# Performance work log

Hardware: AMD Instinct MI355X
Metric: run time of the kernel (lower is better)

Reference implementation:

```python
import jax, jax.numpy as jnp
import numpy as np

EPS = 1e-06
MAX_R = 18.0
TINY = 1e-15

D_MODEL = 512
H = 8
N_SP = 32          # spatial_dim per head
A = N_SP + 1       # Lorentz ambient dim
TAU = 1.0
KARCHER_STEPS = 1
B, T = 2, 512


def minkowski_inner(x, y):
    # <x,y>_L = -x0*y0 + sum_i xi*yi
    return -x[..., 0] * y[..., 0] + jnp.sum(x[..., 1:] * y[..., 1:], axis=-1)


def project_to_hyperboloid(x):
    xx = jnp.maximum(jnp.abs(minkowski_inner(x, x)), TINY)
    y = x / jnp.sqrt(xx)[..., None]
    return jnp.concatenate([jnp.abs(y[..., :1]), y[..., 1:]], axis=-1)


def FL(z):
    # Euclidean param z in R^n -> Lorentz point in H^n (R^{n+1})
    r = jnp.linalg.norm(z, axis=-1, keepdims=True)
    r_safe = jnp.clip(r, 1e-12, MAX_R)
    s = z / r_safe
    y = jnp.concatenate([jnp.cosh(r_safe), jnp.sinh(r_safe) * s], axis=-1)
    return project_to_hyperboloid(y)


def safe_acosh(z):
    return jnp.arccosh(jnp.maximum(z, 1.0 + EPS))


def log_map(p, y):
    alpha = -minkowski_inner(p, y)                       # (...,)
    dist = safe_acosh(alpha)[..., None]                  # (...,1)
    u = y + alpha[..., None] * p
    un = jnp.sqrt(jnp.maximum(minkowski_inner(u, u), TINY))[..., None]
    return (dist / jnp.maximum(un, TINY)) * u


def exp_map(p, v):
    vn = jnp.sqrt(jnp.maximum(minkowski_inner(v, v), TINY))[..., None]
    y = jnp.cosh(vn) * p + (jnp.sinh(vn) / jnp.maximum(vn, TINY)) * v
    return project_to_hyperboloid(y)


def _forward(x, Wq, bq, Wk, bk, Wv, bv, Wo, bo):
    Bx, Tx, _ = x.shape

    def lift(W, b):
        z = x @ W.T + b                                   # (B,T,H*n)
        return z.reshape(Bx, Tx, H, N_SP).transpose(0, 2, 1, 3)  # (B,H,T,n)

    Q = FL(lift(Wq, bq))                                  # (B,H,T,A)
    K = FL(lift(Wk, bk))
    V = FL(lift(Wv, bv))

    # pairwise hyperbolic distance: -<Q_i,K_j>_L = Q0*K0 - spatial dot
    ip = (jnp.einsum('bhi,bhj->bhij', Q[..., 0], K[..., 0])
          - jnp.einsum('bhia,bhja->bhij', Q[..., 1:], K[..., 1:]))
    d = safe_acosh(ip)                                    # (B,H,T,T)
    scores = -TAU * d * d
    attn = jax.nn.softmax(scores, axis=-1)                # (B,H,T,T)

    # Karcher-mean aggregation of V around Y (init at Q)
    Y = Q
    for _ in range(KARCHER_STEPS):
        logv = log_map(Y[:, :, :, None, :], V[:, :, None, :, :])  # (B,H,T,T,A)
        u = jnp.einsum('bhij,bhija->bhia', attn, logv)            # (B,H,T,A)
        Y = exp_map(Y, u)

    # log-map at origin anchor, project to d_model
    Y_bTHA = Y.transpose(0, 2, 1, 3)                      # (B,T,H,A)
    p0 = jnp.zeros((A,), dtype=Y.dtype).at[0].set(1.0)    # Lorentz origin
    Z_tan = log_map(jnp.broadcast_to(p0, Y_bTHA.shape), Y_bTHA)
    Z_tan = Z_tan.reshape(Bx, Tx, H * A)
    Z = Z_tan @ Wo.T + bo                                 # (B,T,d_model)
    return Z


def setup_inputs() -> dict:
    key = jax.random.key(0)
    ks = jax.random.split(key, 9)
    sc = 0.02
    return {
        'x':  jax.random.normal(ks[0], (B, T, D_MODEL), dtype=jnp.float32),
        'Wq': jax.random.normal(ks[1], (H * N_SP, D_MODEL), dtype=jnp.float32) * sc,
        'bq': jnp.zeros((H * N_SP,), dtype=jnp.float32),
        'Wk': jax.random.normal(ks[2], (H * N_SP, D_MODEL), dtype=jnp.float32) * sc,
        'bk': jnp.zeros((H * N_SP,), dtype=jnp.float32),
        'Wv': jax.random.normal(ks[3], (H * N_SP, D_MODEL), dtype=jnp.float32) * sc,
        'bv': jnp.zeros((H * N_SP,), dtype=jnp.float32),
        'Wo': jax.random.normal(ks[4], (D_MODEL, H * A), dtype=jnp.float32) * sc,
        'bo': jnp.zeros((D_MODEL,), dtype=jnp.float32),
    }


def reference(x, Wq, bq, Wk, bk, Wv, bv, Wo, bo):
    return _forward(x, Wq, bq, Wk, bk, Wv, bv, Wo, bo)
```

## Files before the change

### kernel.cpp

```cpp
#include <hip/hip_runtime.h>
#include <math.h>


namespace {

constexpr int Tq = 512;
constexpr int QS = 36;

#define EPSF  1e-6f
#define CINV  3.16227766e7f

using short8 = __attribute__((ext_vector_type(8))) short;
using f32x4  = __attribute__((ext_vector_type(4))) float;

__device__ __forceinline__ float facosh(float x) {
    return __logf(x + __builtin_amdgcn_sqrtf(fmaf(x, x, -1.0f)));
}

__device__ __forceinline__ void cvt_hilo(float x, unsigned short& h, unsigned short& l) {
    const unsigned u = __float_as_uint(x);
    h = (unsigned short)(u >> 16);
    const float xh = __uint_as_float(u & 0xFFFF0000u);
    l = (unsigned short)(__float_as_uint(x - xh) >> 16);
}

__device__ __forceinline__ unsigned short cvt_rne(float x) {
    const unsigned u = __float_as_uint(x);
    return (unsigned short)((u + 0x7FFFu + ((u >> 16) & 1u)) >> 16);
}

__device__ __forceinline__ uint4 pack8(const unsigned short* s) {
    uint4 r;
    r.x = (unsigned)s[0] | ((unsigned)s[1] << 16);
    r.y = (unsigned)s[2] | ((unsigned)s[3] << 16);
    r.z = (unsigned)s[4] | ((unsigned)s[5] << 16);
    r.w = (unsigned)s[6] | ((unsigned)s[7] << 16);
    return r;
}

__global__ __launch_bounds__(256) void gemm_qkv_mfma_kernel(
    const float* __restrict__ x,
    const float* __restrict__ Wq, const float* __restrict__ bq,
    const float* __restrict__ Wk, const float* __restrict__ bk,
    const float* __restrict__ Wv, const float* __restrict__ bv,
    float* __restrict__ Qf, unsigned short* __restrict__ Qh,
    unsigned short* __restrict__ Kh,
    unsigned short* __restrict__ Vh, unsigned short* __restrict__ V2h)
{
    __shared__ unsigned short Ah[16][72];
    __shared__ unsigned short Bh[64][72];
    __shared__ float sT[16][65];

    const int bid = blockIdx.y * 12 + blockIdx.x;
    const int swz = (bid & 7) * 96 + (bid >> 3);
    const int n0 = (swz >> 6) * 64;
    const int m0 = (swz & 63) * 16;

    const int t  = threadIdx.x;
    const int l  = t & 63, w = t >> 6;
    const int wc = w * 16;
    const int fr = l & 15, fk = (l >> 4) * 8;

    const int arow = t >> 4, akseg = (t & 15) * 4;
    const int brow = t >> 2, bkseg = (t & 3) * 16;
    const int ob  = n0 + brow;
    const float* WselB = (ob < 256) ? Wq : (ob < 512 ? Wk : Wv);
    const int obr = ob & 255;

    f32x4 acc = (f32x4){0.f, 0.f, 0.f, 0.f};

    for (int k0 = 0; k0 < 512; k0 += 64) {
        {
            const float4 av = *reinterpret_cast<const float4*>(
                &x[(m0 + arow) * 512 + k0 + akseg]);
            uint2 H;
            H.x = (unsigned)cvt_rne(av.x) | ((unsigned)cvt_rne(av.y) << 16);
            H.y = (unsigned)cvt_rne(av.z) | ((unsigned)cvt_rne(av.w) << 16);
            *reinterpret_cast<uint2*>(&Ah[arow][akseg]) = H;

            const float* wp = WselB + obr * 512 + k0 + bkseg;
            unsigned short hh[16];
            #pragma unroll
            for (int c = 0; c < 4; ++c) {
                const float4 v = *reinterpret_cast<const float4*>(wp + c * 4);
                hh[c*4+0] = cvt_rne(v.x); hh[c*4+1] = cvt_rne(v.y);
                hh[c*4+2] = cvt_rne(v.z); hh[c*4+3] = cvt_rne(v.w);
            }
            *reinterpret_cast<uint4*>(&Bh[brow][bkseg])     = pack8(hh);
            *reinterpret_cast<uint4*>(&Bh[brow][bkseg + 8]) = pack8(hh + 8);
        }
        __syncthreads();

        #pragma unroll
        for (int ks = 0; ks < 2; ++ks) {
            const int kb = ks * 32 + fk;
            const short8 ah = *reinterpret_cast<const short8*>(&Ah[fr][kb]);
            const short8 bh = *reinterpret_cast<const short8*>(&Bh[wc + fr][kb]);
            acc = __builtin_amdgcn_mfma_f32_16x16x32_bf16(ah, bh, acc, 0, 0, 0);
        }
        __syncthreads();
    }

    #pragma unroll
    for (int r = 0; r < 4; ++r)
        sT[(l >> 4) * 4 + r][wc + fr] = acc[r];
    __syncthreads();

    if (t < 32) {
        const int m = t >> 1, half = t & 1;
        const int row = m0 + m;
        const int b = row >> 9, tt = row & 511;
        const int which = n0 >> 8;
        const int h = ((n0 & 255) >> 5) + half;
        const int bh2 = b * 8 + h;
        const float* bsel = (which == 0) ? bq : (which == 1 ? bk : bv);

        float ys[32];
        float s2 = 0.f;
        #pragma unroll
        for (int k = 0; k < 32; ++k) {
            ys[k] = sT[m][half * 32 + k] + bsel[h * 32 + k];
            s2 = fmaf(ys[k], ys[k], s2);
        }
        const float rr = __builtin_amdgcn_sqrtf(s2);
        const float rs = fminf(fmaxf(rr, 1e-12f), 18.0f);
        const float e  = __expf(rs);
        const float ei = __builtin_amdgcn_rcpf(e);
        const float ch = 0.5f * (e + ei);
        float sc = 0.5f * (e - ei) / rs;
        if (rs < 1e-3f) sc = fmaf(rs * rs, 1.0f / 6.0f, 1.0f);
        float y0 = ch;
        float mink = -y0 * y0;
        #pragma unroll
        for (int k = 0; k < 32; ++k) { ys[k] *= sc; mink = fmaf(ys[k], ys[k], mink); }
        const float inv = __builtin_amdgcn_rsqf(fmaxf(fabsf(mink), 1e-15f));
        y0 = fabsf(y0 * inv);

        const long rbase = (long)(bh2 * Tq + tt) * 64;
        unsigned short hbuf[64];
        #pragma unroll
        for (int k = 33; k < 64; ++k) hbuf[k] = 0;

        if (which == 0) {
            float* qp = Qf + (bh2 * Tq + tt) * QS;
            #pragma unroll
            for (int c = 0; c < 8; ++c) {
                float4 v4;
                v4.x = ys[c*4+0] * inv; v4.y = ys[c*4+1] * inv;
                v4.z = ys[c*4+2] * inv; v4.w = ys[c*4+3] * inv;
                *reinterpret_cast<float4*>(qp + c * 4) = v4;
                hbuf[c*4+0] = cvt_rne(v4.x); hbuf[c*4+1] = cvt_rne(v4.y);
                hbuf[c*4+2] = cvt_rne(v4.z); hbuf[c*4+3] = cvt_rne(v4.w);
            }
            float4 tail; tail.x = y0; tail.y = 0.f; tail.z = 0.f; tail.w = 0.f;
            *reinterpret_cast<float4*>(qp + 32) = tail;
            hbuf[32] = cvt_rne(y0);
            #pragma unroll
            for (int c = 0; c < 8; ++c)
                *reinterpret_cast<uint4*>(&Qh[rbase + c * 8]) = pack8(hbuf + c * 8);
        } else if (which == 1) {
            #pragma unroll
            for (int k = 0; k < 32; ++k)
                hbuf[k] = cvt_rne(-ys[k] * inv);
            hbuf[32] = cvt_rne(y0);
            #pragma unroll
            for (int c = 0; c < 8; ++c)
                *reinterpret_cast<uint4*>(&Kh[rbase + c * 8]) = pack8(hbuf + c * 8);
        } else {
            const long v2b = (long)bh2 * 48 * Tq + tt;
            #pragma unroll
            for (int k = 0; k < 32; ++k) {
                const float v = ys[k] * inv;
                hbuf[k] = cvt_rne(-v);
                V2h[v2b + (1 + k) * Tq] = cvt_rne(v);
            }
            hbuf[32] = cvt_rne(y0);
            V2h[v2b] = cvt_rne(y0);
            #pragma unroll
            for (int c = 0; c < 8; ++c)
                *reinterpret_cast<uint4*>(&Vh[rbase + c * 8]) = pack8(hbuf + c * 8);
        }
    }
}

__global__ __launch_bounds__(512) void attn_mfma_kernel(
    const float* __restrict__ Qf, const unsigned short* __restrict__ Qh,
    const unsigned short* __restrict__ Kh,
    const unsigned short* __restrict__ Vh, const unsigned short* __restrict__ V2h,
    float* __restrict__ Ztan)
{
    __shared__ unsigned short sPh[16][528];
    __shared__ float sSe[8][16];
    __shared__ float sWp[2][16][48];

    const int bid = blockIdx.y * 32 + blockIdx.x;
    const int swz = (bid & 7) * 64 + (bid >> 3);
    const int bh = swz >> 5;
    const int i0 = (swz & 31) * 16;

    const int t  = threadIdx.x;
    const int l  = t & 63, w = t >> 6;
    const int fr = l & 15, fk = (l >> 4) * 8;

    short8 qh[2];
    {
        const long qb = (long)(bh * Tq + i0 + fr) * 64;
        #pragma unroll
        for (int ks = 0; ks < 2; ++ks)
            qh[ks] = *reinterpret_cast<const short8*>(&Qh[qb + ks * 32 + fk]);
    }

    float seLoc[4] = {0.f, 0.f, 0.f, 0.f};
    #pragma unroll
    for (int c = 0; c < 4; ++c) {
        const int j0 = (w * 4 + c) * 16;
        const long kb = (long)(bh * Tq + j0 + fr) * 64;
        f32x4 aK = (f32x4){0.f, 0.f, 0.f, 0.f};
        f32x4 aV = (f32x4){0.f, 0.f, 0.f, 0.f};
        #pragma unroll
        for (int ks = 0; ks < 2; ++ks) {
            const long o = kb + ks * 32 + fk;
            const short8 bkh = *reinterpret_cast<const short8*>(&Kh[o]);
            const short8 bvh = *reinterpret_cast<const short8*>(&Vh[o]);
            aK = __builtin_amdgcn_mfma_f32_16x16x32_bf16(qh[ks], bkh, aK, 0, 0, 0);
            aV = __builtin_amdgcn_mfma_f32_16x16x32_bf16(qh[ks], bvh, aV, 0, 0, 0);
        }
        #pragma unroll
        for (int r = 0; r < 4; ++r) {
            const int i = (l >> 4) * 4 + r;
            const int j = j0 + fr;
            const float d  = facosh(fmaxf(aK[r], 1.0f + EPSF));
            const float al = fmaxf(aV[r], 1.0f + EPSF);
            const float e  = __expf(-d * d);
            const float p  = e * facosh(al);
            seLoc[r] += e;
            sPh[i][j] = cvt_rne(p);
        }
    }
    #pragma unroll
    for (int r = 0; r < 4; ++r) {
        float v = seLoc[r];
        v += __shfl_xor(v, 1, 64);
        v += __shfl_xor(v, 2, 64);
        v += __shfl_xor(v, 4, 64);
        v += __shfl_xor(v, 8, 64);
        if ((l & 15) == 0) sSe[w][(l >> 4) * 4 + r] = v;
    }
    __syncthreads();

    if (w < 6) {
        const int a0  = (w % 3) * 16;
        const int kh2 = w / 3;
        const long vb = (long)bh * 48 * Tq + (long)(a0 + fr) * Tq;
        f32x4 aW = (f32x4){0.f, 0.f, 0.f, 0.f};
        #pragma unroll 4
        for (int ks = kh2 * 8; ks < kh2 * 8 + 8; ++ks) {
            const int ko = ks * 32 + fk;
            const short8 ph  = *reinterpret_cast<const short8*>(&sPh[fr][ko]);
            const short8 v2h = *reinterpret_cast<const short8*>(&V2h[vb + ko]);
            aW = __builtin_amdgcn_mfma_f32_16x16x32_bf16(ph, v2h, aW, 0, 0, 0);
        }
        #pragma unroll
        for (int r = 0; r < 4; ++r)
            sWp[kh2][(l >> 4) * 4 + r][a0 + fr] = aW[r];
    }
    __syncthreads();

    if (t < 16) {
        const int i = t;
        float seT = 0.f;
        #pragma unroll
        for (int ww = 0; ww < 8; ++ww) seT += sSe[ww][i];
        float W[33];
        #pragma unroll
        for (int a = 0; a < 33; ++a) W[a] = sWp[0][i][a] + sWp[1][i][a];
        const float* qrow = Qf + (long)(bh * Tq + i0 + i) * QS;
        const float q0 = qrow[32];
        float dot = 0.f;
        #pragma unroll
        for (int a = 1; a < 33; ++a) dot = fmaf(qrow[a - 1], W[a], dot);
        const float S = q0 * W[0] - dot;
        const float cs = CINV * __builtin_amdgcn_rcpf(seT);
        const float y0 = fmaf(cs, fmaf(S, q0, W[0]), q0);
        float mink = -y0 * y0;
        float yv[32];
        #pragma unroll
        for (int a = 1; a < 33; ++a) {
            const float qa = qrow[a - 1];
            const float ya = fmaf(cs, fmaf(S, qa, W[a]), qa);
            yv[a - 1] = ya;
            mink = fmaf(ya, ya, mink);
        }
        const float inv = __builtin_amdgcn_rsqf(fmaxf(fabsf(mink), 1e-15f));
        const float Y0 = fabsf(y0 * inv);
        const float dist0 = facosh(fmaxf(Y0, 1.0f + EPSF));
        const float coef = dist0 * CINV;
        const int b = bh >> 3, h = bh & 7;
        float* zp = Ztan + ((b * Tq + (i0 + i)) * 264) + h * 33;
        zp[0] = coef * (2.0f * Y0);
        #pragma unroll
        for (int a = 1; a < 33; ++a) zp[a] = coef * (yv[a - 1] * inv);
    }
}

__global__ __launch_bounds__(256) void out_gemm_mfma_kernel(
    const float* __restrict__ Ztan, const float* __restrict__ Wo,
    const float* __restrict__ bo, float* __restrict__ out)
{
    __shared__ unsigned short Ah[32][72], Al[32][72];
    __shared__ unsigned short Bh[32][72], Bl[32][72];

    const int n0 = blockIdx.x * 32;
    const int m0 = blockIdx.y * 32;
    const int t  = threadIdx.x;
    const int l  = t & 63, w = t >> 6;
    const int wr = (w >> 1) * 16, wc = (w & 1) * 16;
    const int fr = l & 15, fk = (l >> 4) * 8;

    const int sr = t >> 3, sk = (t & 7) * 8;

    f32x4 acc = (f32x4){0.f, 0.f, 0.f, 0.f};

    for (int k0 = 0; k0 < 264; k0 += 64) {
        const bool full = (k0 + sk + 7 < 264);
        {
            unsigned short h8[8], l8[8];
            if (full) {
                const float4 a0v = *reinterpret_cast<const float4*>(
                    &Ztan[(m0 + sr) * 264 + k0 + sk]);
                const float4 a1v = *reinterpret_cast<const float4*>(
                    &Ztan[(m0 + sr) * 264 + k0 + sk + 4]);
                cvt_hilo(a0v.x, h8[0], l8[0]); cvt_hilo(a0v.y, h8[1], l8[1]);
                cvt_hilo(a0v.z, h8[2], l8[2]); cvt_hilo(a0v.w, h8[3], l8[3]);
                cvt_hilo(a1v.x, h8[4], l8[4]); cvt_hilo(a1v.y, h8[5], l8[5]);
                cvt_hilo(a1v.z, h8[6], l8[6]); cvt_hilo(a1v.w, h8[7], l8[7]);
            } else {
                #pragma unroll
                for (int c = 0; c < 8; ++c) { h8[c] = 0; l8[c] = 0; }
            }
            *reinterpret_cast<uint4*>(&Ah[sr][sk]) = pack8(h8);
            *reinterpret_cast<uint4*>(&Al[sr][sk]) = pack8(l8);

            if (full) {
                const float4 b0v = *reinterpret_cast<const float4*>(
                    &Wo[(n0 + sr) * 264 + k0 + sk]);
                const float4 b1v = *reinterpret_cast<const float4*>(
                    &Wo[(n0 + sr) * 264 + k0 + sk + 4]);
                cvt_hilo(b0v.x, h8[0], l8[0]); cvt_hilo(b0v.y, h8[1], l8[1]);
                cvt_hilo(b0v.z, h8[2], l8[2]); cvt_hilo(b0v.w, h8[3], l8[3]);
                cvt_hilo(b1v.x, h8[4], l8[4]); cvt_hilo(b1v.y, h8[5], l8[5]);
                cvt_hilo(b1v.z, h8[6], l8[6]); cvt_hilo(b1v.w, h8[7], l8[7]);
            } else {
                #pragma unroll
                for (int c = 0; c < 8; ++c) { h8[c] = 0; l8[c] = 0; }
            }
            *reinterpret_cast<uint4*>(&Bh[sr][sk]) = pack8(h8);
            *reinterpret_cast<uint4*>(&Bl[sr][sk]) = pack8(l8);
        }
        __syncthreads();

        #pragma unroll
        for (int ks = 0; ks < 2; ++ks) {
            const int kb = ks * 32 + fk;
            const short8 ah  = *reinterpret_cast<const short8*>(&Ah[wr + fr][kb]);
            const short8 al_ = *reinterpret_cast<const short8*>(&Al[wr + fr][kb]);
            const short8 bh  = *reinterpret_cast<const short8*>(&Bh[wc + fr][kb]);
            const short8 bl_ = *reinterpret_cast<const short8*>(&Bl[wc + fr][kb]);
            acc = __builtin_amdgcn_mfma_f32_16x16x32_bf16(ah, bh, acc, 0, 0, 0);
            acc = __builtin_amdgcn_mfma_f32_16x16x32_bf16(ah, bl_, acc, 0, 0, 0);
            acc = __builtin_amdgcn_mfma_f32_16x16x32_bf16(al_, bh, acc, 0, 0, 0);
        }
        __syncthreads();
    }

    const int col = n0 + wc + fr;
    const float bias = bo[col];
    #pragma unroll
    for (int r = 0; r < 4; ++r) {
        const int row = m0 + wr + (l >> 4) * 4 + r;
        out[row * 512 + col] = acc[r] + bias;
    }
}

}

extern "C" void kernel_launch(void* const* d_in, const int* in_sizes, int n_in,
                              void* d_out, int out_size, void* d_ws, size_t ws_size,
                              hipStream_t stream)
{
    const float* x  = (const float*)d_in[0];
    const float* Wq = (const float*)d_in[1];
    const float* bq = (const float*)d_in[2];
    const float* Wk = (const float*)d_in[3];
    const float* bk = (const float*)d_in[4];
    const float* Wv = (const float*)d_in[5];
    const float* bv = (const float*)d_in[6];
    const float* Wo = (const float*)d_in[7];
    const float* bo = (const float*)d_in[8];
    float* out = (float*)d_out;

    float* ws = (float*)d_ws;
    float* Qf = ws;
    unsigned short* Qh  = (unsigned short*)(ws + 294912);
    unsigned short* Kh  = (unsigned short*)(ws + 557056);
    unsigned short* Vh  = (unsigned short*)(ws + 819200);
    unsigned short* V2h = (unsigned short*)(ws + 1081344);
    float* Zt = ws + 1277952;

    gemm_qkv_mfma_kernel<<<dim3(12, 64), 256, 0, stream>>>(
        x, Wq, bq, Wk, bk, Wv, bv, Qf, Qh, Kh, Vh, V2h);
    attn_mfma_kernel<<<dim3(32, 16), 512, 0, stream>>>(
        Qf, Qh, Kh, Vh, V2h, Zt);
    out_gemm_mfma_kernel<<<dim3(16, 32), 256, 0, stream>>>(Zt, Wo, bo, out);
}
```

Measured before the change: 37.30 us.

## Load MFMA fragments directly from global memory, bypassing LDS staging in GEMMs

Both the QKV projection GEMM and the output GEMM now have each lane read its MFMA operand fragment straight from global memory and convert it to bf16 in registers. This removes the shared-memory staging tiles and the two __syncthreads per K step. In exchange, each operand element is loaded redundantly by every wave that needs it, which leans on L1/L2 for reuse and uses less coalesced per-lane row loads. The output GEMM's K loop is now fully unrolled with a zero-padded tail step.

```diff
diff --git a/kernel.cpp b/kernel.cpp
--- a/kernel.cpp
+++ b/kernel.cpp
@@ -36,6 +36,29 @@
     r.z = (unsigned)s[4] | ((unsigned)s[5] << 16);
     r.w = (unsigned)s[6] | ((unsigned)s[7] << 16);
     return r;
+}
+
+__device__ __forceinline__ short8 frag_rne(const float* p) {
+    const float4 a = *reinterpret_cast<const float4*>(p);
+    const float4 b = *reinterpret_cast<const float4*>(p + 4);
+    unsigned short s[8];
+    s[0] = cvt_rne(a.x); s[1] = cvt_rne(a.y); s[2] = cvt_rne(a.z); s[3] = cvt_rne(a.w);
+    s[4] = cvt_rne(b.x); s[5] = cvt_rne(b.y); s[6] = cvt_rne(b.z); s[7] = cvt_rne(b.w);
+    const uint4 u = pack8(s);
+    return *reinterpret_cast<const short8*>(&u);
+}
+
+__device__ __forceinline__ void frag_hilo(const float* p, short8& hi, short8& lo) {
+    const float4 a = *reinterpret_cast<const float4*>(p);
+    const float4 b = *reinterpret_cast<const float4*>(p + 4);
+    unsigned short h[8], l[8];
+    cvt_hilo(a.x, h[0], l[0]); cvt_hilo(a.y, h[1], l[1]);
+    cvt_hilo(a.z, h[2], l[2]); cvt_hilo(a.w, h[3], l[3]);
+    cvt_hilo(b.x, h[4], l[4]); cvt_hilo(b.y, h[5], l[5]);
+    cvt_hilo(b.z, h[6], l[6]); cvt_hilo(b.w, h[7], l[7]);
+    const uint4 uh = pack8(h), ul = pack8(l);
+    hi = *reinterpret_cast<const short8*>(&uh);
+    lo = *reinterpret_cast<const short8*>(&ul);
 }
 
 __global__ __launch_bounds__(256) void gemm_qkv_mfma_kernel(
@@ -47,8 +70,6 @@
     unsigned short* __restrict__ Kh,
     unsigned short* __restrict__ Vh, unsigned short* __restrict__ V2h)
 {
-    __shared__ unsigned short Ah[16][72];
-    __shared__ unsigned short Bh[64][72];
     __shared__ float sT[16][65];
 
     const int bid = blockIdx.y * 12 + blockIdx.x;
@@ -61,44 +82,21 @@
     const int wc = w * 16;
     const int fr = l & 15, fk = (l >> 4) * 8;
 
-    const int arow = t >> 4, akseg = (t & 15) * 4;
-    const int brow = t >> 2, bkseg = (t & 3) * 16;
-    const int ob  = n0 + brow;
-    const float* WselB = (ob < 256) ? Wq : (ob < 512 ? Wk : Wv);
-    const int obr = ob & 255;
+    const int which = n0 >> 8;
+    const float* Wsel = (which == 0) ? Wq : (which == 1 ? Wk : Wv);
+    const int obr = (n0 & 255) + wc + fr;
+
+    const float* xrow = x + (m0 + fr) * 512;
+    const float* wrow = Wsel + obr * 512;
 
     f32x4 acc = (f32x4){0.f, 0.f, 0.f, 0.f};
 
-    for (int k0 = 0; k0 < 512; k0 += 64) {
-        {
-            const float4 av = *reinterpret_cast<const float4*>(
-                &x[(m0 + arow) * 512 + k0 + akseg]);
-            uint2 H;
-            H.x = (unsigned)cvt_rne(av.x) | ((unsigned)cvt_rne(av.y) << 16);
-            H.y = (unsigned)cvt_rne(av.z) | ((unsigned)cvt_rne(av.w) << 16);
-            *reinterpret_cast<uint2*>(&Ah[arow][akseg]) = H;
-
-            const float* wp = WselB + obr * 512 + k0 + bkseg;
-            unsigned short hh[16];
-            #pragma unroll
-            for (int c = 0; c < 4; ++c) {
-                const float4 v = *reinterpret_cast<const float4*>(wp + c * 4);
-                hh[c*4+0] = cvt_rne(v.x); hh[c*4+1] = cvt_rne(v.y);
-                hh[c*4+2] = cvt_rne(v.z); hh[c*4+3] = cvt_rne(v.w);
-            }
-            *reinterpret_cast<uint4*>(&Bh[brow][bkseg])     = pack8(hh);
-            *reinterpret_cast<uint4*>(&Bh[brow][bkseg + 8]) = pack8(hh + 8);
-        }
-        __syncthreads();
-
-        #pragma unroll
-        for (int ks = 0; ks < 2; ++ks) {
-            const int kb = ks * 32 + fk;
-            const short8 ah = *reinterpret_cast<const short8*>(&Ah[fr][kb]);
-            const short8 bh = *reinterpret_cast<const short8*>(&Bh[wc + fr][kb]);
-            acc = __builtin_amdgcn_mfma_f32_16x16x32_bf16(ah, bh, acc, 0, 0, 0);
-        }
-        __syncthreads();
+    #pragma unroll 4
+    for (int ks = 0; ks < 16; ++ks) {
+        const int kb = ks * 32 + fk;
+        const short8 ah = frag_rne(xrow + kb);
+        const short8 bh = frag_rne(wrow + kb);
+        acc = __builtin_amdgcn_mfma_f32_16x16x32_bf16(ah, bh, acc, 0, 0, 0);
     }
 
     #pragma unroll
@@ -110,7 +108,6 @@
         const int m = t >> 1, half = t & 1;
         const int row = m0 + m;
         const int b = row >> 9, tt = row & 511;
-        const int which = n0 >> 8;
         const int h = ((n0 & 255) >> 5) + half;
         const int bh2 = b * 8 + h;
         const float* bsel = (which == 0) ? bq : (which == 1 ? bk : bv);
@@ -307,9 +304,6 @@
     const float* __restrict__ Ztan, const float* __restrict__ Wo,
     const float* __restrict__ bo, float* __restrict__ out)
 {
-    __shared__ unsigned short Ah[32][72], Al[32][72];
-    __shared__ unsigned short Bh[32][72], Bl[32][72];
-
     const int n0 = blockIdx.x * 32;
     const int m0 = blockIdx.y * 32;
     const int t  = threadIdx.x;
@@ -317,60 +311,25 @@
     const int wr = (w >> 1) * 16, wc = (w & 1) * 16;
     const int fr = l & 15, fk = (l >> 4) * 8;
 
-    const int sr = t >> 3, sk = (t & 7) * 8;
+    const float* arow = Ztan + (m0 + wr + fr) * 264;
+    const float* brow = Wo + (n0 + wc + fr) * 264;
 
     f32x4 acc = (f32x4){0.f, 0.f, 0.f, 0.f};
 
-    for (int k0 = 0; k0 < 264; k0 += 64) {
-        const bool full = (k0 + sk + 7 < 264);
-        {
-            unsigned short h8[8], l8[8];
-            if (full) {
-                const float4 a0v = *reinterpret_cast<const float4*>(
-                    &Ztan[(m0 + sr) * 264 + k0 + sk]);
-                const float4 a1v = *reinterpret_cast<const float4*>(
-                    &Ztan[(m0 + sr) * 264 + k0 + sk + 4]);
-                cvt_hilo(a0v.x, h8[0], l8[0]); cvt_hilo(a0v.y, h8[1], l8[1]);
-                cvt_hilo(a0v.z, h8[2], l8[2]); cvt_hilo(a0v.w, h8[3], l8[3]);
-                cvt_hilo(a1v.x, h8[4], l8[4]); cvt_hilo(a1v.y, h8[5], l8[5]);
-                cvt_hilo(a1v.z, h8[6], l8[6]); cvt_hilo(a1v.w, h8[7], l8[7]);
-            } else {
-                #pragma unroll
-                for (int c = 0; c < 8; ++c) { h8[c] = 0; l8[c] = 0; }
-            }
-            *reinterpret_cast<uint4*>(&Ah[sr][sk]) = pack8(h8);
-            *reinterpret_cast<uint4*>(&Al[sr][sk]) = pack8(l8);
-
-            if (full) {
-                const float4 b0v = *reinterpret_cast<const float4*>(
-                    &Wo[(n0 + sr) * 264 + k0 + sk]);
-                const float4 b1v = *reinterpret_cast<const float4*>(
-                    &Wo[(n0 + sr) * 264 + k0 + sk + 4]);
-                cvt_hilo(b0v.x, h8[0], l8[0]); cvt_hilo(b0v.y, h8[1], l8[1]);
-                cvt_hilo(b0v.z, h8[2], l8[2]); cvt_hilo(b0v.w, h8[3], l8[3]);
-                cvt_hilo(b1v.x, h8[4], l8[4]); cvt_hilo(b1v.y, h8[5], l8[5]);
-                cvt_hilo(b1v.z, h8[6], l8[6]); cvt_hilo(b1v.w, h8[7], l8[7]);
-            } else {
-                #pragma unroll
-                for (int c = 0; c < 8; ++c) { h8[c] = 0; l8[c] = 0; }
-            }
-            *reinterpret_cast<uint4*>(&Bh[sr][sk]) = pack8(h8);
-            *reinterpret_cast<uint4*>(&Bl[sr][sk]) = pack8(l8);
-        }
-        __syncthreads();
-
-        #pragma unroll
-        for (int ks = 0; ks < 2; ++ks) {
-            const int kb = ks * 32 + fk;
-            const short8 ah  = *reinterpret_cast<const short8*>(&Ah[wr + fr][kb]);
-            const short8 al_ = *reinterpret_cast<const short8*>(&Al[wr + fr][kb]);
-            const short8 bh  = *reinterpret_cast<const short8*>(&Bh[wc + fr][kb]);
-            const short8 bl_ = *reinterpret_cast<const short8*>(&Bl[wc + fr][kb]);
-            acc = __builtin_amdgcn_mfma_f32_16x16x32_bf16(ah, bh, acc, 0, 0, 0);
-            acc = __builtin_amdgcn_mfma_f32_16x16x32_bf16(ah, bl_, acc, 0, 0, 0);
-            acc = __builtin_amdgcn_mfma_f32_16x16x32_bf16(al_, bh, acc, 0, 0, 0);
-        }
-        __syncthreads();
+    #pragma unroll
+    for (int ks = 0; ks < 9; ++ks) {
+        const int kb = ks * 32 + fk;
+        short8 ah, al_, bh, bl_;
+        if (kb + 8 <= 264) {
+            frag_hilo(arow + kb, ah, al_);
+            frag_hilo(brow + kb, bh, bl_);
+        } else {
+            const short8 z = (short8){0, 0, 0, 0, 0, 0, 0, 0};
+            ah = z; al_ = z; bh = z; bl_ = z;
+        }
+        acc = __builtin_amdgcn_mfma_f32_16x16x32_bf16(ah, bh, acc, 0, 0, 0);
+        acc = __builtin_amdgcn_mfma_f32_16x16x32_bf16(ah, bl_, acc, 0, 0, 0);
+        acc = __builtin_amdgcn_mfma_f32_16x16x32_bf16(al_, bh, acc, 0, 0, 0);
     }
 
     const int col = n0 + wc + fr;
```

After: 52.31 us. 1.4x slower.
